# Kernel tuning notes

Hardware: AMD Instinct MI355X
Metric: run time of the kernel (lower is better)

## Reference

```python
import jax, jax.numpy as jnp
import numpy as np

DIM = 1024
HEADS = 16
HEAD_DIM = DIM // HEADS
HIDDEN = 4096  # mlp_ratio * dim
SCALE = HEAD_DIM ** -0.5
LN_EPS = 1e-5


def softmax_one(x):
    # softmax with +1 in the denominator (after max subtraction), per source
    m = jnp.max(x, axis=-1, keepdims=True)
    e = jnp.exp(x - m)
    return e / (1.0 + jnp.sum(e, axis=-1, keepdims=True))


def layer_norm(x, g, b):
    mu = jnp.mean(x, axis=-1, keepdims=True)
    var = jnp.mean(jnp.square(x - mu), axis=-1, keepdims=True)
    return (x - mu) * jax.lax.rsqrt(var + LN_EPS) * g + b


def setup_inputs() -> dict:
    key = jax.random.key(0)
    ks = jax.random.split(key, 12)
    B, C, N = 2, DIM, 2048
    x = jax.random.normal(ks[0], (B, C, N), dtype=jnp.float32)
    mask = jax.random.randint(ks[1], (B, HEADS, N), 0, 2, dtype=jnp.int32)
    s = 0.02
    return {
        'x': x,
        'mask': mask,
        'qkv_w': jax.random.normal(ks[2], (3 * DIM, DIM), jnp.float32) * s,
        'qkv_b': jnp.zeros((3 * DIM,), jnp.float32),
        'proj_w': jax.random.normal(ks[3], (DIM, DIM), jnp.float32) * s,
        'proj_b': jnp.zeros((DIM,), jnp.float32),
        'fc1_w': jax.random.normal(ks[4], (HIDDEN, DIM), jnp.float32) * s,
        'fc1_b': jnp.zeros((HIDDEN,), jnp.float32),
        'ln_g': jnp.ones((HIDDEN,), jnp.float32),
        'ln_b': jnp.zeros((HIDDEN,), jnp.float32),
        'fc2_w': jax.random.normal(ks[5], (DIM, HIDDEN), jnp.float32) * s,
        'fc2_b': jnp.zeros((DIM,), jnp.float32),
    }


def reference(x, mask, qkv_w, qkv_b, proj_w, proj_b, fc1_w, fc1_b, ln_g, ln_b, fc2_w, fc2_b):
    B, C, N = x.shape
    xt = jnp.swapaxes(x, 1, 2)  # (B, N, C)

    # ----- attention -----
    qkv = xt @ qkv_w.T + qkv_b                      # (B, N, 3C)
    qkv = qkv.reshape(B, N, 3, HEADS, HEAD_DIM)
    qkv = jnp.transpose(qkv, (2, 0, 3, 1, 4))       # (3, B, H, N, Dh)
    q, k, v = qkv[0], qkv[1], qkv[2]
    scores = jnp.einsum('bhnd,bhmd->bhnm', q * SCALE, k)  # (B, H, N, N)
    scores = jnp.where(mask[:, :, :, None] == 0, -1e9, scores)
    attn = softmax_one(scores)
    out = jnp.einsum('bhnm,bhmd->bhnd', attn, v)    # (B, H, N, Dh)
    # faithful to source: permute(0,3,1,2).reshape(B,N,C) -> scrambled merge
    out = jnp.transpose(out, (0, 3, 1, 2)).reshape(B, N, C)
    out = out @ proj_w.T + proj_b

    # faithful residual: attn_out + ls1(attn_out) with ls1 = Identity
    h = out + out                                   # (B, N, C)

    # ----- MLP (timm Mlp: fc1 -> GELU -> LayerNorm -> fc2) -----
    m = h @ fc1_w.T + fc1_b
    m = jax.nn.gelu(m, approximate=False)
    m = layer_norm(m, ln_g, ln_b)
    m = m @ fc2_w.T + fc2_b
    y = h + m                                       # (B, N, C)

    return jnp.swapaxes(y, 1, 2)                    # (B, C, N)
```

## Files before the change

### kernel.cpp

```cpp
#include <hip/hip_runtime.h>
#include <math.h>

#define DIMC   1024
#define NTOK   2048
#define BATCH  2
#define HEADS  16
#define HDIM   64
#define HIDDEN 4096
#define MROWS  (BATCH*NTOK)
#define QSZ    ((size_t)BATCH*HEADS*NTOK*HDIM)
#define QSC    0.18033688f

typedef unsigned short ushort_t;
typedef __attribute__((ext_vector_type(8))) short short8;
typedef __attribute__((ext_vector_type(4))) float f32x4;
typedef __attribute__((ext_vector_type(4))) unsigned short us4;

__device__ __forceinline__ ushort_t f2b(float f) {
  union { float f; unsigned int u; } cv; cv.f = f;
  unsigned int u = cv.u;
  unsigned int r = (u + 0x7fffu + ((u >> 16) & 1u)) >> 16;
  return (ushort_t)r;
}

__device__ __forceinline__ float b2f(ushort_t b) {
  union { unsigned int u; float f; } cv; cv.u = ((unsigned int)b) << 16;
  return cv.f;
}

__device__ __forceinline__ float fexp2(float x) {
#if __has_builtin(__builtin_amdgcn_exp2f)
  return __builtin_amdgcn_exp2f(x);
#else
  return exp2f(x);
#endif
}

__device__ __forceinline__ void gl_lds16(const void* g, void* l) {
  __builtin_amdgcn_global_load_lds(
      (const __attribute__((address_space(1))) void*)g,
      (__attribute__((address_space(3))) void*)l, 16, 0, 0);
}

__device__ __forceinline__ void lds_barrier() {
  __builtin_amdgcn_s_waitcnt(0xC07F);
  __builtin_amdgcn_s_barrier();
}

__global__ __launch_bounds__(256) void k_transpose(const float* __restrict__ x,
                                                   ushort_t* __restrict__ xt) {
  __shared__ float t[32][33];
  int b  = blockIdx.z;
  int c0 = blockIdx.y * 32, n0 = blockIdx.x * 32;
  int tx = threadIdx.x, ty = threadIdx.y;
#pragma unroll
  for (int l = 0; l < 4; l++)
    t[ty + l * 8][tx] = x[((size_t)(b * DIMC + c0 + ty + l * 8)) * NTOK + n0 + tx];
  __syncthreads();
#pragma unroll
  for (int l = 0; l < 4; l++)
    xt[((size_t)(b * NTOK + n0 + ty + l * 8)) * DIMC + c0 + tx] = f2b(t[tx][ty + l * 8]);
}

__global__ __launch_bounds__(256) void k_f2b4(const float* __restrict__ w0,
                                              const float* __restrict__ w1,
                                              const float* __restrict__ w2,
                                              const float* __restrict__ w3,
                                              ushort_t* __restrict__ o0,
                                              ushort_t* __restrict__ o1,
                                              ushort_t* __restrict__ o2,
                                              ushort_t* __restrict__ o3) {
  int bid = blockIdx.x;
  const float* in; ushort_t* out; int base;
  if (bid < 3072)      { in = w0; out = o0; base = bid; }
  else if (bid < 4096) { in = w1; out = o1; base = bid - 3072; }
  else if (bid < 8192) { in = w2; out = o2; base = bid - 4096; }
  else                 { in = w3; out = o3; base = bid - 8192; }
  int i = base * 256 + threadIdx.x;
  float4 v = ((const float4*)in)[i];
  us4 o; o.x = f2b(v.x); o.y = f2b(v.y); o.z = f2b(v.z); o.w = f2b(v.w);
  ((us4*)out)[i] = o;
}

template <int EPI, int NTX8, int KSTRIDE, int KLEN>
__global__ __launch_bounds__(256) void k_gemm_bf16(const ushort_t* __restrict__ A,
                                                   const ushort_t* __restrict__ W,
                                                   const float* __restrict__ bias,
                                                   void* __restrict__ outv) {
  __shared__ ushort_t As[2][128 * 32];
  __shared__ ushort_t Bs[2][128 * 32];
  const int tid = threadIdx.x;
  const int lane = tid & 63, wv = tid >> 6;
  const int bid = blockIdx.x, kz = blockIdx.y;
  const int xcd = bid & 7, t = bid >> 3;
  const int row0 = (t / NTX8) * 128;
  const int col0 = (xcd * NTX8 + (t % NTX8)) * 128;
  const int wrow0 = (wv >> 1) * 64, wcol0 = (wv & 1) * 64;
  const int lm = lane & 15, lq = lane >> 4;
  const int srow = wv * 32 + (lane >> 2);
  const int gch = (lane & 3) ^ ((lane >> 3) & 3);
  const int sslot = (lane & 3) * 8;
  const int sw8 = (lq ^ ((lm >> 1) & 3)) * 8;

  const ushort_t* Ab = A + (size_t)(row0 + srow) * KSTRIDE + (size_t)kz * KLEN + gch * 8;
  const ushort_t* Wb = W + (size_t)(col0 + srow) * KSTRIDE + (size_t)kz * KLEN + gch * 8;
  const size_t rstep = (size_t)16 * KSTRIDE;

  short8 ga0[2], gb0[2], ga1[2], gb1[2];

  f32x4 acc[4][4];
#pragma unroll
  for (int i = 0; i < 4; i++)
#pragma unroll
    for (int j = 0; j < 4; j++) acc[i][j] = (f32x4){0.f, 0.f, 0.f, 0.f};

#define GLOAD(sl, k0) do {                                     \
    ga##sl[0] = *(const short8*)(Ab + (k0));                   \
    ga##sl[1] = *(const short8*)(Ab + rstep + (k0));           \
    gb##sl[0] = *(const short8*)(Wb + (k0));                   \
    gb##sl[1] = *(const short8*)(Wb + rstep + (k0));           \
  } while (0)
#define SWRITE(buf, sl) do {                                   \
    *(short8*)&As[buf][srow * 32 + sslot]        = ga##sl[0];  \
    *(short8*)&As[buf][(srow + 16) * 32 + sslot] = ga##sl[1];  \
    *(short8*)&Bs[buf][srow * 32 + sslot]        = gb##sl[0];  \
    *(short8*)&Bs[buf][(srow + 16) * 32 + sslot] = gb##sl[1];  \
  } while (0)

  auto compute = [&](int buf) {
    short8 af[4], bf[4];
#pragma unroll
    for (int mi = 0; mi < 4; mi++)
      af[mi] = *(const short8*)&As[buf][(wrow0 + mi * 16 + lm) * 32 + sw8];
#pragma unroll
    for (int ni = 0; ni < 4; ni++)
      bf[ni] = *(const short8*)&Bs[buf][(wcol0 + ni * 16 + lm) * 32 + sw8];
#pragma unroll
    for (int mi = 0; mi < 4; mi++)
#pragma unroll
      for (int ni = 0; ni < 4; ni++)
        acc[mi][ni] = __builtin_amdgcn_mfma_f32_16x16x32_bf16(af[mi], bf[ni], acc[mi][ni], 0, 0, 0);
  };

  constexpr int S = KLEN / 32;
  GLOAD(0, 0);
  GLOAD(1, 32);
  SWRITE(0, 0);

#pragma unroll 1
  for (int kk = 0; kk < S; kk += 2) {
    lds_barrier();
    if (kk + 2 < S) GLOAD(0, (kk + 2) * 32);
    SWRITE(1, 1);
    compute(0);
    lds_barrier();
    if (kk + 3 < S) GLOAD(1, (kk + 3) * 32);
    if (kk + 2 < S) SWRITE(0, 0);
    compute(1);
  }
#undef GLOAD
#undef SWRITE

#pragma unroll
  for (int mi = 0; mi < 4; mi++) {
#pragma unroll
    for (int ni = 0; ni < 4; ni++) {
#pragma unroll
      for (int r = 0; r < 4; r++) {
        const int row = row0 + wrow0 + mi * 16 + lq * 4 + r;
        const int col = col0 + wcol0 + ni * 16 + lm;
        float v = acc[mi][ni][r];
        if (EPI != 4) v += bias[col];
        if (EPI == 0) {
          int which = col >> 10, rem = col & 1023, hh = rem >> 6, d = rem & 63;
          int bb = row >> 11, n = row & 2047;
          size_t bh = (size_t)(bb * HEADS + hh);
          ushort_t* o16 = (ushort_t*)outv;
          if (which == 0)
            o16[(bh * NTOK + n) * HDIM + d] = f2b(v * QSC);
          else if (which == 1)
            o16[QSZ + (bh * NTOK + n) * HDIM + d] = f2b(v);
          else
            o16[2 * QSZ + (bh * HDIM + d) * NTOK + n] = f2b(v);
        } else if (EPI == 2) {
          ((ushort_t*)outv)[(size_t)row * HIDDEN + col] = f2b(v);
        } else {
          ((float*)outv)[(size_t)kz * MROWS * DIMC + (size_t)row * DIMC + col] = v;
        }
      }
    }
  }
}

__global__ __launch_bounds__(256) void k_comb_proj(const float* __restrict__ p0,
                                                   const float* __restrict__ p1,
                                                   const float* __restrict__ bias,
                                                   ushort_t* __restrict__ hb) {
  int i = blockIdx.x * 256 + threadIdx.x;
  int colb = (i & 255) * 4;
  float4 a = ((const float4*)p0)[i];
  float4 b = ((const float4*)p1)[i];
  us4 o;
  o.x = f2b(2.f * (a.x + b.x + bias[colb + 0]));
  o.y = f2b(2.f * (a.y + b.y + bias[colb + 1]));
  o.z = f2b(2.f * (a.z + b.z + bias[colb + 2]));
  o.w = f2b(2.f * (a.w + b.w + bias[colb + 3]));
  ((us4*)hb)[i] = o;
}

__global__ __launch_bounds__(256) void k_comb_fc2(const float* __restrict__ p0,
                                                  const float* __restrict__ p1,
                                                  const ushort_t* __restrict__ hb,
                                                  const float* __restrict__ bias,
                                                  float* __restrict__ out) {
  __shared__ float t[32][33];
  int b  = blockIdx.z;
  int c0 = blockIdx.y * 32, n0 = blockIdx.x * 32;
  int tx = threadIdx.x, ty = threadIdx.y;
#pragma unroll
  for (int l = 0; l < 4; l++) {
    size_t idx = ((size_t)(b * NTOK + n0 + ty + l * 8)) * DIMC + c0 + tx;
    t[ty + l * 8][tx] = p0[idx] + p1[idx] + b2f(hb[idx]) + bias[c0 + tx];
  }
  __syncthreads();
#pragma unroll
  for (int l = 0; l < 4; l++)
    out[((size_t)(b * DIMC + c0 + ty + l * 8)) * NTOK + n0 + tx] = t[tx][ty + l * 8];
}

__global__ __launch_bounds__(256) void k_attn_mfma(const ushort_t* __restrict__ qkv,
                                                   const int* __restrict__ mask,
                                                   ushort_t* __restrict__ scram) {
  __shared__ ushort_t Kl[2][64 * 64];
  __shared__ ushort_t Vl[2][64 * 64];
  __shared__ ushort_t Pl[4 * 32 * 72];
  const int tid = threadIdx.x;
  const int lane = tid & 63, w = tid >> 6;
  const int lm = lane & 15, quad = lane >> 4;
  const int bh = blockIdx.y, b = bh >> 4, h = bh & 15;
  const int q0 = blockIdx.x * 128 + w * 32;
  const ushort_t* qg  = qkv + (size_t)bh * NTOK * HDIM;
  const ushort_t* kg  = qkv + QSZ + (size_t)bh * NTOK * HDIM;
  const ushort_t* vTg = qkv + 2 * QSZ + (size_t)bh * HDIM * NTOK;
  ushort_t* Pw = &Pl[w * 32 * 72];

  const short8 ones = {0x3F80, 0x3F80, 0x3F80, 0x3F80, 0x3F80, 0x3F80, 0x3F80, 0x3F80};

  short8 qf[2][2];
#pragma unroll
  for (int qs = 0; qs < 2; qs++)
#pragma unroll
    for (int hf = 0; hf < 2; hf++)
      qf[qs][hf] = *(const short8*)&qg[(size_t)(q0 + qs * 16 + lm) * HDIM + hf * 32 + quad * 8];

  bool mk[2][4];
#pragma unroll
  for (int qs = 0; qs < 2; qs++)
#pragma unroll
    for (int r = 0; r < 4; r++)
      mk[qs][r] = mask[(size_t)bh * NTOK + q0 + qs * 16 + quad * 4 + r] != 0;

  f32x4 O[2][4], La[2];
#pragma unroll
  for (int qs = 0; qs < 2; qs++) {
    La[qs] = (f32x4){0.f, 0.f, 0.f, 0.f};
#pragma unroll
    for (int r = 0; r < 4; r++) O[qs][r] = (f32x4){0.f, 0.f, 0.f, 0.f};
  }

  const int s0 = tid, s1 = tid + 256;
  const int r0 = s0 >> 3, g0 = (s0 & 7) ^ (r0 & 7);
  const int r1 = s1 >> 3, g1 = (s1 & 7) ^ (r1 & 7);

  gl_lds16(kg + (size_t)r0 * HDIM + g0 * 8, &Kl[0][s0 * 8]);
  gl_lds16(kg + (size_t)r1 * HDIM + g1 * 8, &Kl[0][s1 * 8]);
  gl_lds16(vTg + (size_t)r0 * NTOK + g0 * 8, &Vl[0][s0 * 8]);
  gl_lds16(vTg + (size_t)r1 * NTOK + g1 * 8, &Vl[0][s1 * 8]);

  for (int kt = 0; kt < NTOK; kt += 64) {
    const int cur = (kt >> 6) & 1, nxt = cur ^ 1;
    __syncthreads();
    if (kt + 64 < NTOK) {
      gl_lds16(kg + (size_t)(kt + 64 + r0) * HDIM + g0 * 8, &Kl[nxt][s0 * 8]);
      gl_lds16(kg + (size_t)(kt + 64 + r1) * HDIM + g1 * 8, &Kl[nxt][s1 * 8]);
      gl_lds16(vTg + (size_t)r0 * NTOK + kt + 64 + g0 * 8, &Vl[nxt][s0 * 8]);
      gl_lds16(vTg + (size_t)r1 * NTOK + kt + 64 + g1 * 8, &Vl[nxt][s1 * 8]);
    }

    short8 kf[4][2];
#pragma unroll
    for (int ksub = 0; ksub < 4; ksub++)
#pragma unroll
      for (int hf = 0; hf < 2; hf++)
        kf[ksub][hf] = *(const short8*)&Kl[cur][(ksub * 16 + lm) * 64 + ((4 * hf + quad) ^ (lm & 7)) * 8];

#pragma unroll
    for (int qs = 0; qs < 2; qs++) {
      f32x4 S[4];
#pragma unroll
      for (int ksub = 0; ksub < 4; ksub++) {
        S[ksub] = (f32x4){0.f, 0.f, 0.f, 0.f};
        S[ksub] = __builtin_amdgcn_mfma_f32_16x16x32_bf16(qf[qs][0], kf[ksub][0], S[ksub], 0, 0, 0);
        S[ksub] = __builtin_amdgcn_mfma_f32_16x16x32_bf16(qf[qs][1], kf[ksub][1], S[ksub], 0, 0, 0);
      }
#pragma unroll
      for (int r = 0; r < 4; r++) {
        const int prow = qs * 16 + quad * 4 + r;
#pragma unroll
        for (int ksub = 0; ksub < 4; ksub++) {
          float p = mk[qs][r] ? fexp2(S[ksub][r]) : 1.0f;
          Pw[prow * 72 + ksub * 16 + lm] = (ushort_t)(__float_as_uint(p) >> 16);
        }
      }
    }
    __builtin_amdgcn_s_waitcnt(0xC07F);

    short8 vf[4][2];
#pragma unroll
    for (int dsub = 0; dsub < 4; dsub++)
#pragma unroll
      for (int hf = 0; hf < 2; hf++)
        vf[dsub][hf] = *(const short8*)&Vl[cur][(dsub * 16 + lm) * 64 + ((4 * hf + quad) ^ (lm & 7)) * 8];

#pragma unroll
    for (int qs = 0; qs < 2; qs++) {
      short8 pf[2];
#pragma unroll
      for (int hf = 0; hf < 2; hf++)
        pf[hf] = *(const short8*)&Pw[(qs * 16 + lm) * 72 + hf * 32 + quad * 8];
#pragma unroll
      for (int dsub = 0; dsub < 4; dsub++) {
        O[qs][dsub] = __builtin_amdgcn_mfma_f32_16x16x32_bf16(pf[0], vf[dsub][0], O[qs][dsub], 0, 0, 0);
        O[qs][dsub] = __builtin_amdgcn_mfma_f32_16x16x32_bf16(pf[1], vf[dsub][1], O[qs][dsub], 0, 0, 0);
      }
      La[qs] = __builtin_amdgcn_mfma_f32_16x16x32_bf16(pf[0], ones, La[qs], 0, 0, 0);
      La[qs] = __builtin_amdgcn_mfma_f32_16x16x32_bf16(pf[1], ones, La[qs], 0, 0, 0);
    }
  }

#pragma unroll
  for (int qs = 0; qs < 2; qs++)
#pragma unroll
    for (int r = 0; r < 4; r++) {
      int n = q0 + qs * 16 + quad * 4 + r;
      float inv = 1.f / (1.f + La[qs][r]);
      int n1 = n >> 10, nn0 = n & 1023;
#pragma unroll
      for (int dsub = 0; dsub < 4; dsub++) {
        int d = dsub * 16 + lm;
        int np = d * 32 + h * 2 + n1;
        scram[((size_t)(b * NTOK + np)) * DIMC + nn0] = f2b(O[qs][dsub][r] * inv);
      }
    }
}

__global__ __launch_bounds__(256) void k_ln(ushort_t* __restrict__ mid,
                                            const float* __restrict__ g,
                                            const float* __restrict__ bta) {
  const int row = blockIdx.x;
  ushort_t* p = mid + (size_t)row * HIDDEN;
  const int tid = threadIdx.x;
  float lv[16];
  float s = 0.f, s2 = 0.f;
#pragma unroll
  for (int i = 0; i < 4; i++) {
    us4 u = *(const us4*)&p[tid * 4 + i * 1024];
#pragma unroll
    for (int j = 0; j < 4; j++) {
      float xx = b2f((j == 0) ? u.x : (j == 1) ? u.y : (j == 2) ? u.z : u.w);
      xx = 0.5f * xx * (1.f + erff(xx * 0.70710678118654752f));
      lv[i * 4 + j] = xx;
      s += xx;
      s2 += xx * xx;
    }
  }
#pragma unroll
  for (int off = 32; off > 0; off >>= 1) {
    s += __shfl_down(s, off);
    s2 += __shfl_down(s2, off);
  }
  __shared__ float rs[4], rs2[4];
  if ((tid & 63) == 0) { rs[tid >> 6] = s; rs2[tid >> 6] = s2; }
  __syncthreads();
  float ts = rs[0] + rs[1] + rs[2] + rs[3];
  float ts2 = rs2[0] + rs2[1] + rs2[2] + rs2[3];
  float mu = ts * (1.f / HIDDEN);
  float var = ts2 * (1.f / HIDDEN) - mu * mu;
  float rstd = rsqrtf(var + 1e-5f);
#pragma unroll
  for (int i = 0; i < 4; i++) {
    us4 o;
#pragma unroll
    for (int j = 0; j < 4; j++) {
      int f = tid * 4 + i * 1024 + j;
      float y = (lv[i * 4 + j] - mu) * rstd * g[f] + bta[f];
      ushort_t ob = f2b(y);
      if (j == 0) o.x = ob; else if (j == 1) o.y = ob; else if (j == 2) o.z = ob; else o.w = ob;
    }
    *(us4*)&p[tid * 4 + i * 1024] = o;
  }
}

extern "C" void kernel_launch(void* const* d_in, const int* in_sizes, int n_in,
                              void* d_out, int out_size, void* d_ws, size_t ws_size,
                              hipStream_t stream) {
  const float* x      = (const float*)d_in[0];
  const int*   mask   = (const int*)d_in[1];
  const float* qkv_w  = (const float*)d_in[2];
  const float* qkv_b  = (const float*)d_in[3];
  const float* proj_w = (const float*)d_in[4];
  const float* proj_b = (const float*)d_in[5];
  const float* fc1_w  = (const float*)d_in[6];
  const float* fc1_b  = (const float*)d_in[7];
  const float* ln_g   = (const float*)d_in[8];
  const float* ln_b   = (const float*)d_in[9];
  const float* fc2_w  = (const float*)d_in[10];
  const float* fc2_b  = (const float*)d_in[11];

  char* w = (char*)d_ws;
  ushort_t* qkv16  = (ushort_t*)w;           w += 3 * QSZ * 2;
  ushort_t* xtb    = (ushort_t*)w;           w += (size_t)MROWS * DIMC * 2;
  ushort_t* scramb = (ushort_t*)w;           w += (size_t)MROWS * DIMC * 2;
  ushort_t* hb     = (ushort_t*)w;           w += (size_t)MROWS * DIMC * 2;
  ushort_t* mid    = (ushort_t*)w;           w += (size_t)MROWS * HIDDEN * 2;
  ushort_t* wqkvb  = (ushort_t*)w;           w += (size_t)3 * DIMC * DIMC * 2;
  ushort_t* wprojb = (ushort_t*)w;           w += (size_t)DIMC * DIMC * 2;
  ushort_t* wfc1b  = (ushort_t*)w;           w += (size_t)HIDDEN * DIMC * 2;
  ushort_t* wfc2b  = (ushort_t*)w;           w += (size_t)DIMC * HIDDEN * 2;
  float*    pbuf   = (float*)w;              w += (size_t)2 * MROWS * DIMC * 4;
  float*    pbuf1  = pbuf + (size_t)MROWS * DIMC;

  k_transpose<<<dim3(NTOK / 32, DIMC / 32, BATCH), dim3(32, 8), 0, stream>>>(x, xtb);
  k_f2b4<<<dim3(12288), 256, 0, stream>>>(qkv_w, proj_w, fc1_w, fc2_w,
                                          wqkvb, wprojb, wfc1b, wfc2b);

  k_gemm_bf16<0, 3, DIMC, DIMC><<<dim3(24 * 32), 256, 0, stream>>>(
      xtb, wqkvb, qkv_b, qkv16);
  k_attn_mfma<<<dim3(NTOK / 128, BATCH * HEADS), 256, 0, stream>>>(
      qkv16, mask, scramb);
  k_gemm_bf16<4, 1, DIMC, 512><<<dim3(8 * 32, 2), 256, 0, stream>>>(
      scramb, wprojb, nullptr, pbuf);
  k_comb_proj<<<dim3(4096), 256, 0, stream>>>(pbuf, pbuf1, proj_b, hb);
  k_gemm_bf16<2, 4, DIMC, DIMC><<<dim3(32 * 32), 256, 0, stream>>>(
      hb, wfc1b, fc1_b, mid);
  k_ln<<<dim3(MROWS), 256, 0, stream>>>(mid, ln_g, ln_b);
  k_gemm_bf16<4, 1, HIDDEN, 2048><<<dim3(8 * 32, 2), 256, 0, stream>>>(
      mid, wfc2b, nullptr, pbuf);
  k_comb_fc2<<<dim3(NTOK / 32, DIMC / 32, BATCH), dim3(32, 8), 0, stream>>>(
      pbuf, pbuf1, hb, fc2_b, (float*)d_out);
}
```

Baseline: 391.5 us.

## Stage GEMM tiles via direct global-to-LDS loads and raise MFMA wave priority

The GEMM kernel no longer loads tiles into registers and writes them to LDS. It now uses global_load_lds DMA into a double-buffered LDS tile, with one __syncthreads per k-step. This frees VGPRs and removes the LDS write instructions, at the cost of relying on __syncthreads waitcnt semantics for the async loads. The attention kernel also wraps its MFMA blocks in s_setprio so matrix work gets scheduling priority over other waves.

```diff
diff --git a/kernel.cpp b/kernel.cpp
--- a/kernel.cpp
+++ b/kernel.cpp
@@ -40,11 +40,6 @@
   __builtin_amdgcn_global_load_lds(
       (const __attribute__((address_space(1))) void*)g,
       (__attribute__((address_space(3))) void*)l, 16, 0, 0);
-}
-
-__device__ __forceinline__ void lds_barrier() {
-  __builtin_amdgcn_s_waitcnt(0xC07F);
-  __builtin_amdgcn_s_barrier();
 }
 
 __global__ __launch_bounds__(256) void k_transpose(const float* __restrict__ x,
@@ -99,32 +94,23 @@
   const int lm = lane & 15, lq = lane >> 4;
   const int srow = wv * 32 + (lane >> 2);
   const int gch = (lane & 3) ^ ((lane >> 3) & 3);
-  const int sslot = (lane & 3) * 8;
   const int sw8 = (lq ^ ((lm >> 1) & 3)) * 8;
 
   const ushort_t* Ab = A + (size_t)(row0 + srow) * KSTRIDE + (size_t)kz * KLEN + gch * 8;
   const ushort_t* Wb = W + (size_t)(col0 + srow) * KSTRIDE + (size_t)kz * KLEN + gch * 8;
   const size_t rstep = (size_t)16 * KSTRIDE;
 
-  short8 ga0[2], gb0[2], ga1[2], gb1[2];
-
   f32x4 acc[4][4];
 #pragma unroll
   for (int i = 0; i < 4; i++)
 #pragma unroll
     for (int j = 0; j < 4; j++) acc[i][j] = (f32x4){0.f, 0.f, 0.f, 0.f};
 
-#define GLOAD(sl, k0) do {                                     \
-    ga##sl[0] = *(const short8*)(Ab + (k0));                   \
-    ga##sl[1] = *(const short8*)(Ab + rstep + (k0));           \
-    gb##sl[0] = *(const short8*)(Wb + (k0));                   \
-    gb##sl[1] = *(const short8*)(Wb + rstep + (k0));           \
-  } while (0)
-#define SWRITE(buf, sl) do {                                   \
-    *(short8*)&As[buf][srow * 32 + sslot]        = ga##sl[0];  \
-    *(short8*)&As[buf][(srow + 16) * 32 + sslot] = ga##sl[1];  \
-    *(short8*)&Bs[buf][srow * 32 + sslot]        = gb##sl[0];  \
-    *(short8*)&Bs[buf][(srow + 16) * 32 + sslot] = gb##sl[1];  \
+#define STAGE(buf, k0) do {                                      \
+    gl_lds16(Ab + (k0),         &As[buf][wv * 1024]);            \
+    gl_lds16(Ab + rstep + (k0), &As[buf][wv * 1024 + 512]);      \
+    gl_lds16(Wb + (k0),         &Bs[buf][wv * 1024]);            \
+    gl_lds16(Wb + rstep + (k0), &Bs[buf][wv * 1024 + 512]);      \
   } while (0)
 
   auto compute = [&](int buf) {
@@ -143,23 +129,14 @@
   };
 
   constexpr int S = KLEN / 32;
-  GLOAD(0, 0);
-  GLOAD(1, 32);
-  SWRITE(0, 0);
-
+  STAGE(0, 0);
 #pragma unroll 1
-  for (int kk = 0; kk < S; kk += 2) {
-    lds_barrier();
-    if (kk + 2 < S) GLOAD(0, (kk + 2) * 32);
-    SWRITE(1, 1);
-    compute(0);
-    lds_barrier();
-    if (kk + 3 < S) GLOAD(1, (kk + 3) * 32);
-    if (kk + 2 < S) SWRITE(0, 0);
-    compute(1);
-  }
-#undef GLOAD
-#undef SWRITE
+  for (int kk = 0; kk < S; kk++) {
+    __syncthreads();
+    if (kk + 1 < S) STAGE((kk + 1) & 1, (kk + 1) * 32);
+    compute(kk & 1);
+  }
+#undef STAGE
 
 #pragma unroll
   for (int mi = 0; mi < 4; mi++) {
@@ -297,12 +274,14 @@
 #pragma unroll
     for (int qs = 0; qs < 2; qs++) {
       f32x4 S[4];
+      __builtin_amdgcn_s_setprio(1);
 #pragma unroll
       for (int ksub = 0; ksub < 4; ksub++) {
         S[ksub] = (f32x4){0.f, 0.f, 0.f, 0.f};
         S[ksub] = __builtin_amdgcn_mfma_f32_16x16x32_bf16(qf[qs][0], kf[ksub][0], S[ksub], 0, 0, 0);
         S[ksub] = __builtin_amdgcn_mfma_f32_16x16x32_bf16(qf[qs][1], kf[ksub][1], S[ksub], 0, 0, 0);
       }
+      __builtin_amdgcn_s_setprio(0);
 #pragma unroll
       for (int r = 0; r < 4; r++) {
         const int prow = qs * 16 + quad * 4 + r;
@@ -328,6 +307,7 @@
 #pragma unroll
       for (int hf = 0; hf < 2; hf++)
         pf[hf] = *(const short8*)&Pw[(qs * 16 + lm) * 72 + hf * 32 + quad * 8];
+      __builtin_amdgcn_s_setprio(1);
 #pragma unroll
       for (int dsub = 0; dsub < 4; dsub++) {
         O[qs][dsub] = __builtin_amdgcn_mfma_f32_16x16x32_bf16(pf[0], vf[dsub][0], O[qs][dsub], 0, 0, 0);
@@ -335,6 +315,7 @@
       }
       La[qs] = __builtin_amdgcn_mfma_f32_16x16x32_bf16(pf[0], ones, La[qs], 0, 0, 0);
       La[qs] = __builtin_amdgcn_mfma_f32_16x16x32_bf16(pf[1], ones, La[qs], 0, 0, 0);
+      __builtin_amdgcn_s_setprio(0);
     }
   }
 
```

Result: no change. 389.6 us (-0.5%).
